# Kernel tuning notes

Measured on AMD Instinct MI355X. Metric: run time of the kernel, lower is better.

Reference implementation:

```python
import jax, jax.numpy as jnp
import numpy as np

N_NODES = 100000
N_EDGES = 1600000
F_IN = 128
HID = 64
N_LAYERS = 4
N_GRAPHS = 512
N_CLASSES = 10
BN_EPS = 1e-5


def setup_inputs() -> dict:
    key = jax.random.key(0)
    ks = jax.random.split(key, 24)
    inp = {
        "x": jax.random.normal(ks[0], (N_NODES, F_IN), dtype=jnp.float32),
        "edge_index": jax.random.randint(ks[1], (2, N_EDGES), 0, N_NODES, dtype=jnp.int32),
        "batch": jnp.sort(jax.random.randint(ks[2], (N_NODES,), 0, N_GRAPHS, dtype=jnp.int32)),
        # GINConv eps (train_eps=True, init 0) per layer
        "eps": jnp.zeros((N_LAYERS,), dtype=jnp.float32),
        # layer 0 MLP (in=F_IN)
        "W1_0": jax.random.normal(ks[3], (F_IN, HID)) * 0.05,
        "b1_0": jnp.zeros((HID,)),
        "g_0": jnp.ones((HID,)),
        "be_0": jnp.zeros((HID,)),
        "W2_0": jax.random.normal(ks[4], (HID, HID)) * 0.05,
        "b2_0": jnp.zeros((HID,)),
        # layers 1..3 MLPs stacked (in=HID)
        "W1_r": jax.random.normal(ks[5], (N_LAYERS - 1, HID, HID)) * 0.05,
        "b1_r": jnp.zeros((N_LAYERS - 1, HID)),
        "g_r": jnp.ones((N_LAYERS - 1, HID)),
        "be_r": jnp.zeros((N_LAYERS - 1, HID)),
        "W2_r": jax.random.normal(ks[6], (N_LAYERS - 1, HID, HID)) * 0.05,
        "b2_r": jnp.zeros((N_LAYERS - 1, HID)),
        # head
        "lin1_W": jax.random.normal(ks[7], (N_LAYERS * HID, HID)) * 0.05,
        "lin1_b": jnp.zeros((HID,)),
        "bn_g": jnp.ones((HID,)),
        "bn_b": jnp.zeros((HID,)),
        "lin2_W": jax.random.normal(ks[8], (HID, N_CLASSES)) * 0.05,
        "lin2_b": jnp.zeros((N_CLASSES,)),
    }
    return inp


def _bn(h, g, b):
    # BatchNorm1d training-mode math: biased variance over the batch dim
    mu = h.mean(axis=0)
    var = h.var(axis=0)
    return (h - mu) * jax.lax.rsqrt(var + BN_EPS) * g + b


def _gin_conv(x, src, dst, eps, W1, b1, g, be, W2, b2):
    # sum of neighbor (source) features scattered to target nodes
    agg = jax.ops.segment_sum(x[src], dst, num_segments=N_NODES)
    h = (1.0 + eps) * x + agg
    h = jax.nn.relu(_bn(h @ W1 + b1, g, be))
    h = jax.nn.relu(h @ W2 + b2)
    return h


def reference(x, edge_index, batch, eps,
              W1_0, b1_0, g_0, be_0, W2_0, b2_0,
              W1_r, b1_r, g_r, be_r, W2_r, b2_r,
              lin1_W, lin1_b, bn_g, bn_b, lin2_W, lin2_b):
    src, dst = edge_index[0], edge_index[1]
    h = _gin_conv(x, src, dst, eps[0], W1_0, b1_0, g_0, be_0, W2_0, b2_0)
    xs = [h]
    for i in range(N_LAYERS - 1):
        h = _gin_conv(h, src, dst, eps[i + 1], W1_r[i], b1_r[i], g_r[i], be_r[i], W2_r[i], b2_r[i])
        xs.append(h)
    hcat = jnp.concatenate(xs, axis=-1)                      # [N, L*HID]
    pooled = jax.ops.segment_sum(hcat, batch, num_segments=N_GRAPHS)  # [G, L*HID]
    out = pooled @ lin1_W + lin1_b
    out = jax.nn.relu(_bn(out, bn_g, bn_b))
    # dropout: eval mode (identity)
    out = out @ lin2_W + lin2_b
    return jax.nn.log_softmax(out, axis=-1)
```

## Files before the change

kernel.cpp:

```cpp
#include <hip/hip_runtime.h>

#define N_NODES 100000
#define N_EDGES 1600000
#define F_IN 128
#define HID 64
#define NLAYERS 4
#define N_GRAPHS 512
#define N_CLASSES 10

#define NB_BUCKET 256
#define NODES_PER_BUCKET 391
#define NBLK 256
#define EDGES_PER_BLK (N_EDGES / NBLK)

typedef unsigned int uint_t;
typedef unsigned short ushort_t;

__device__ __forceinline__ float lo_bf(uint_t w) { return __uint_as_float(w << 16); }
__device__ __forceinline__ float hi_bf(uint_t w) { return __uint_as_float(w & 0xffff0000u); }
__device__ __forceinline__ ushort_t f2bf(float f) {
    uint_t u = __float_as_uint(f);
    u += 0x7fffu + ((u >> 16) & 1u);
    return (ushort_t)(u >> 16);
}
__device__ __forceinline__ uint_t pack2(float a, float b) {
    return ((uint_t)f2bf(b) << 16) | (uint_t)f2bf(a);
}

__global__ __launch_bounds__(256) void k_zero(int* __restrict__ btotal,
                                              float* __restrict__ statsA,
                                              float* __restrict__ pooled) {
    int i = blockIdx.x * 256 + threadIdx.x;
    if (i < NB_BUCKET) btotal[i] = 0;
    if (i < NLAYERS * 128) statsA[i] = 0.f;
    if (i < N_GRAPHS * 256) pooled[i] = 0.f;
}

__global__ __launch_bounds__(512) void kb_hist(const int* __restrict__ dst,
                                               int* __restrict__ partial,
                                               int* __restrict__ btotal) {
    __shared__ int h[NB_BUCKET];
    int tid = threadIdx.x;
    if (tid < NB_BUCKET) h[tid] = 0;
    __syncthreads();
    int e0 = blockIdx.x * EDGES_PER_BLK;
    for (int i = tid; i < EDGES_PER_BLK; i += 512) {
        uint_t d = (uint_t)dst[e0 + i];
        if (d >= (uint_t)N_NODES) d = N_NODES - 1;
        atomicAdd(&h[d / NODES_PER_BUCKET], 1);
    }
    __syncthreads();
    if (tid < NB_BUCKET) {
        int c = h[tid];
        partial[blockIdx.x * NB_BUCKET + tid] = c;
        if (c) atomicAdd(&btotal[tid], c);
    }
}

__global__ __launch_bounds__(256) void kb_base(const int* __restrict__ btotal,
                                               int* __restrict__ bbase) {
    __shared__ int sh[NB_BUCKET];
    int tid = threadIdx.x;
    sh[tid] = btotal[tid];
    __syncthreads();
    for (int off = 1; off < NB_BUCKET; off <<= 1) {
        int t = (tid >= off) ? sh[tid - off] : 0;
        __syncthreads();
        sh[tid] += t;
        __syncthreads();
    }
    bbase[tid + 1] = sh[tid];
    if (tid == 0) bbase[0] = 0;
}

__global__ __launch_bounds__(256) void kb_scan(const int* __restrict__ partial,
                                               const int* __restrict__ bbase,
                                               int* __restrict__ goff) {
    __shared__ int sh[NBLK];
    int b = blockIdx.x, tid = threadIdx.x;
    sh[tid] = partial[tid * NB_BUCKET + b];
    __syncthreads();
    for (int off = 1; off < NBLK; off <<= 1) {
        int t = (tid >= off) ? sh[tid - off] : 0;
        __syncthreads();
        sh[tid] += t;
        __syncthreads();
    }
    int excl = (tid == 0) ? 0 : sh[tid - 1];
    goff[tid * NB_BUCKET + b] = bbase[b] + excl;
}

__global__ __launch_bounds__(512) void kb_scatter(const int* __restrict__ src,
                                                  const int* __restrict__ dst,
                                                  const int* __restrict__ goff,
                                                  int* __restrict__ ebuf) {
    __shared__ int cur[NB_BUCKET];
    int tid = threadIdx.x;
    if (tid < NB_BUCKET) cur[tid] = goff[blockIdx.x * NB_BUCKET + tid];
    __syncthreads();
    int e0 = blockIdx.x * EDGES_PER_BLK;
    for (int i = tid; i < EDGES_PER_BLK; i += 512) {
        uint_t d = (uint_t)dst[e0 + i];
        if (d >= (uint_t)N_NODES) d = N_NODES - 1;
        uint_t s = (uint_t)src[e0 + i];
        if (s >= (uint_t)N_NODES) s = 0;
        int b = (int)(d / NODES_PER_BUCKET);
        int dl = (int)d - b * NODES_PER_BUCKET;
        int pos = atomicAdd(&cur[b], 1);
        ebuf[pos] = (dl << 17) | (int)s;
    }
}

__global__ __launch_bounds__(512) void kb_csr(const int* __restrict__ ebuf,
                                              const int* __restrict__ bbase,
                                              int* __restrict__ row_ptr,
                                              int* __restrict__ col_src) {
    __shared__ int cnt[512];
    __shared__ int sh[512];
    __shared__ int off[512];
    int tid = threadIdx.x, b = blockIdx.x;
    int s0 = bbase[b], s1 = bbase[b + 1];
    int n = s1 - s0;
    cnt[tid] = 0;
    __syncthreads();
    for (int i = tid; i < n; i += 512) {
        int dl = ebuf[s0 + i] >> 17;
        atomicAdd(&cnt[dl], 1);
    }
    __syncthreads();
    sh[tid] = cnt[tid];
    __syncthreads();
    for (int o = 1; o < 512; o <<= 1) {
        int t = (tid >= o) ? sh[tid - o] : 0;
        __syncthreads();
        sh[tid] += t;
        __syncthreads();
    }
    off[tid] = (tid == 0) ? 0 : sh[tid - 1];
    cnt[tid] = 0;

    int node0 = b * NODES_PER_BUCKET;
    int ncnt = N_NODES - node0;
    if (ncnt > NODES_PER_BUCKET) ncnt = NODES_PER_BUCKET;
    if (tid < ncnt) row_ptr[node0 + tid] = s0 + off[tid];
    if (b == NB_BUCKET - 1 && tid == 0) row_ptr[N_NODES] = N_EDGES;
    __syncthreads();

    for (int i = tid; i < n; i += 512) {
        int v = ebuf[s0 + i];
        int dl = v >> 17;
        int r = atomicAdd(&cnt[dl], 1);
        col_src[s0 + off[dl] + r] = v & 0x1FFFF;
    }
}

__global__ __launch_bounds__(256) void k_aggregate_u(const uint2* __restrict__ y2,
                                                     const int* __restrict__ row_ptr,
                                                     const int* __restrict__ col_src,
                                                     const float* __restrict__ eps, int layer,
                                                     const float* __restrict__ b1,
                                                     uint2* __restrict__ u2) {
    int wid = threadIdx.x >> 6, lane = threadIdx.x & 63;
    int gid = lane >> 4, l4 = lane & 15;
    float one_eps = 1.0f + eps[layer];
    int stride = gridDim.x * 4;

    for (int node = blockIdx.x * 4 + wid; node < N_NODES; node += stride) {
        int e0 = row_ptr[node], e1 = row_ptr[node + 1];
        if (e0 < 0) e0 = 0;
        if (e1 > N_EDGES) e1 = N_EDGES;
        if (e1 < e0) e1 = e0;

        float4 a0 = {0.f, 0.f, 0.f, 0.f}, a1 = a0, a2 = a0, a3 = a0;

        for (int ebase = e0; ebase < e1; ebase += 64) {
            int len = e1 - ebase; if (len > 64) len = 64;
            int ci = ebase + lane; if (ci > e1 - 1) ci = e1 - 1;
            int sv = col_src[ci];
            sv = (int)min((uint_t)sv, (uint_t)(N_NODES - 1));

            int nfull = len >> 2;
            int rem = len & 3;
            int j = 0;
            for (; j + 4 <= nfull; j += 4) {
                int s0 = __shfl(sv, (j + 0) * 4 + gid, 64);
                int s1 = __shfl(sv, (j + 1) * 4 + gid, 64);
                int s2 = __shfl(sv, (j + 2) * 4 + gid, 64);
                int s3 = __shfl(sv, (j + 3) * 4 + gid, 64);
                uint2 w0 = y2[(size_t)s0 * 16 + l4];
                uint2 w1 = y2[(size_t)s1 * 16 + l4];
                uint2 w2 = y2[(size_t)s2 * 16 + l4];
                uint2 w3 = y2[(size_t)s3 * 16 + l4];
                a0.x += lo_bf(w0.x); a0.y += hi_bf(w0.x); a0.z += lo_bf(w0.y); a0.w += hi_bf(w0.y);
                a1.x += lo_bf(w1.x); a1.y += hi_bf(w1.x); a1.z += lo_bf(w1.y); a1.w += hi_bf(w1.y);
                a2.x += lo_bf(w2.x); a2.y += hi_bf(w2.x); a2.z += lo_bf(w2.y); a2.w += hi_bf(w2.y);
                a3.x += lo_bf(w3.x); a3.y += hi_bf(w3.x); a3.z += lo_bf(w3.y); a3.w += hi_bf(w3.y);
            }
            for (; j < nfull; ++j) {
                int s = __shfl(sv, j * 4 + gid, 64);
                uint2 w = y2[(size_t)s * 16 + l4];
                a0.x += lo_bf(w.x); a0.y += hi_bf(w.x); a0.z += lo_bf(w.y); a0.w += hi_bf(w.y);
            }
            if (rem) {
                int s = __shfl(sv, nfull * 4 + gid, 64);
                if (gid < rem) {
                    uint2 w = y2[(size_t)s * 16 + l4];
                    a1.x += lo_bf(w.x); a1.y += hi_bf(w.x); a1.z += lo_bf(w.y); a1.w += hi_bf(w.y);
                }
            }
        }

        float4 t;
        t.x = (a0.x + a1.x) + (a2.x + a3.x);
        t.y = (a0.y + a1.y) + (a2.y + a3.y);
        t.z = (a0.z + a1.z) + (a2.z + a3.z);
        t.w = (a0.w + a1.w) + (a2.w + a3.w);
        t.x += __shfl_xor(t.x, 16, 64); t.x += __shfl_xor(t.x, 32, 64);
        t.y += __shfl_xor(t.y, 16, 64); t.y += __shfl_xor(t.y, 32, 64);
        t.z += __shfl_xor(t.z, 16, 64); t.z += __shfl_xor(t.z, 32, 64);
        t.w += __shfl_xor(t.w, 16, 64); t.w += __shfl_xor(t.w, 32, 64);

        if (gid == 0) {
            uint2 ws = y2[(size_t)node * 16 + l4];
            float4 bb = *(const float4*)&b1[4 * l4];
            float ox = t.x + one_eps * lo_bf(ws.x) + bb.x;
            float oy = t.y + one_eps * hi_bf(ws.x) + bb.y;
            float oz = t.z + one_eps * lo_bf(ws.y) + bb.z;
            float ow = t.w + one_eps * hi_bf(ws.y) + bb.w;
            uint2 o2;
            o2.x = pack2(ox, oy);
            o2.y = pack2(oz, ow);
            u2[(size_t)node * 16 + l4] = o2;
        }
    }
}

template <int K>
__global__ __launch_bounds__(256) void k_gemm1(const float* __restrict__ A,
                                               const float* __restrict__ W,
                                               ushort_t* __restrict__ out) {
    constexpr int KP = K + 4;
    constexpr int KQ = K / 4;
    __shared__ float Al[64 * KP];
    __shared__ float Wl[K * 64];
    int tid = threadIdx.x;
    int base = blockIdx.x * 64;

    for (int i = tid; i < K * 16; i += 256)
        ((float4*)Wl)[i] = ((const float4*)W)[i];

    if (base + 64 <= N_NODES) {
        const float4* Ag = (const float4*)(A + (size_t)base * K);
        for (int i = tid; i < 16 * K; i += 256) {
            int row = i / KQ, kk = (i % KQ) * 4;
            float4 v = Ag[i];
            *(float4*)&Al[row * KP + kk] = v;
        }
    } else {
        for (int i = tid; i < 16 * K; i += 256) {
            int row = i / KQ, kk = (i % KQ) * 4;
            int grow = base + row; if (grow >= N_NODES) grow = N_NODES - 1;
            float4 v = ((const float4*)(A + (size_t)grow * K))[i % KQ];
            *(float4*)&Al[row * KP + kk] = v;
        }
    }
    __syncthreads();

    int ct = (tid & 15) * 4;
    int rb = (tid >> 4) * 4;
    float4 acc0 = {0.f, 0.f, 0.f, 0.f}, acc1 = acc0, acc2 = acc0, acc3 = acc0;
    const float* A0 = &Al[(rb + 0) * KP];
    const float* A1 = &Al[(rb + 1) * KP];
    const float* A2 = &Al[(rb + 2) * KP];
    const float* A3 = &Al[(rb + 3) * KP];
    #pragma unroll 4
    for (int k = 0; k < K; ++k) {
        float4 w = *(const float4*)&Wl[k * 64 + ct];
        float a0 = A0[k], a1 = A1[k], a2 = A2[k], a3 = A3[k];
        acc0.x = fmaf(a0, w.x, acc0.x); acc0.y = fmaf(a0, w.y, acc0.y);
        acc0.z = fmaf(a0, w.z, acc0.z); acc0.w = fmaf(a0, w.w, acc0.w);
        acc1.x = fmaf(a1, w.x, acc1.x); acc1.y = fmaf(a1, w.y, acc1.y);
        acc1.z = fmaf(a1, w.z, acc1.z); acc1.w = fmaf(a1, w.w, acc1.w);
        acc2.x = fmaf(a2, w.x, acc2.x); acc2.y = fmaf(a2, w.y, acc2.y);
        acc2.z = fmaf(a2, w.z, acc2.z); acc2.w = fmaf(a2, w.w, acc2.w);
        acc3.x = fmaf(a3, w.x, acc3.x); acc3.y = fmaf(a3, w.y, acc3.y);
        acc3.z = fmaf(a3, w.z, acc3.z); acc3.w = fmaf(a3, w.w, acc3.w);
    }

    float4 accs[4] = {acc0, acc1, acc2, acc3};
    #pragma unroll
    for (int r = 0; r < 4; ++r) {
        int row = base + rb + r;
        if (row < N_NODES) {
            ushort4 o;
            o.x = f2bf(accs[r].x); o.y = f2bf(accs[r].y);
            o.z = f2bf(accs[r].z); o.w = f2bf(accs[r].w);
            *(ushort4*)&out[(size_t)row * 64 + ct] = o;
        }
    }
}

template <bool NEXT>
__global__ __launch_bounds__(256) void k_fused(const uint2* __restrict__ U2,
                                               const float* __restrict__ W2,
                                               const float* __restrict__ sums,
                                               const float* __restrict__ g_,
                                               const float* __restrict__ be,
                                               const float* __restrict__ b2,
                                               const int* __restrict__ batch,
                                               float* __restrict__ pooled, int layer,
                                               const float* __restrict__ W1n,
                                               ushort_t* __restrict__ ynext) {
    constexpr int K = 64, KP = 68, KQ = 16;
    __shared__ float Al[64 * KP];
    __shared__ float Wl[K * 64];
    __shared__ float W1l[NEXT ? K * 64 : 4];
    __shared__ float Pl[256];
    __shared__ __align__(16) float Sc[64];
    __shared__ __align__(16) float Sh[64];
    int tid = threadIdx.x;
    int base = blockIdx.x * 64;

    if (tid < 64) {
        const float inv_n = 1.0f / N_NODES;
        float mean = sums[tid] * inv_n;
        float var = sums[64 + tid] * inv_n - mean * mean;
        if (var < 0.f) var = 0.f;
        float inv = rsqrtf(var + 1e-5f);
        float sc = inv * g_[tid];
        Sc[tid] = sc;
        Sh[tid] = be[tid] - mean * sc;
    }
    for (int i = tid; i < K * 16; i += 256)
        ((float4*)Wl)[i] = ((const float4*)W2)[i];
    if (NEXT) {
        for (int i = tid; i < K * 16; i += 256)
            ((float4*)W1l)[i] = ((const float4*)W1n)[i];
    }
    __syncthreads();

    {
        bool full = (base + 64 <= N_NODES);
        for (int i = tid; i < 16 * K; i += 256) {
            int row = i / KQ, kq = i % KQ, kk = kq * 4;
            int grow = base + row;
            if (!full && grow >= N_NODES) grow = N_NODES - 1;
            uint2 w = U2[(size_t)grow * 16 + kq];
            float4 v = {lo_bf(w.x), hi_bf(w.x), lo_bf(w.y), hi_bf(w.y)};
            float4 sc = *(const float4*)&Sc[kk];
            float4 sh = *(const float4*)&Sh[kk];
            v.x = fmaxf(fmaf(v.x, sc.x, sh.x), 0.f);
            v.y = fmaxf(fmaf(v.y, sc.y, sh.y), 0.f);
            v.z = fmaxf(fmaf(v.z, sc.z, sh.z), 0.f);
            v.w = fmaxf(fmaf(v.w, sc.w, sh.w), 0.f);
            *(float4*)&Al[row * KP + kk] = v;
        }
    }
    __syncthreads();

    int ct = (tid & 15) * 4;
    int rb = (tid >> 4) * 4;
    float4 acc0 = {0.f, 0.f, 0.f, 0.f}, acc1 = acc0, acc2 = acc0, acc3 = acc0;
    {
        const float* A0 = &Al[(rb + 0) * KP];
        const float* A1 = &Al[(rb + 1) * KP];
        const float* A2 = &Al[(rb + 2) * KP];
        const float* A3 = &Al[(rb + 3) * KP];
        #pragma unroll 4
        for (int k = 0; k < K; ++k) {
            float4 w = *(const float4*)&Wl[k * 64 + ct];
            float a0 = A0[k], a1 = A1[k], a2 = A2[k], a3 = A3[k];
            acc0.x = fmaf(a0, w.x, acc0.x); acc0.y = fmaf(a0, w.y, acc0.y);
            acc0.z = fmaf(a0, w.z, acc0.z); acc0.w = fmaf(a0, w.w, acc0.w);
            acc1.x = fmaf(a1, w.x, acc1.x); acc1.y = fmaf(a1, w.y, acc1.y);
            acc1.z = fmaf(a1, w.z, acc1.z); acc1.w = fmaf(a1, w.w, acc1.w);
            acc2.x = fmaf(a2, w.x, acc2.x); acc2.y = fmaf(a2, w.y, acc2.y);
            acc2.z = fmaf(a2, w.z, acc2.z); acc2.w = fmaf(a2, w.w, acc2.w);
            acc3.x = fmaf(a3, w.x, acc3.x); acc3.y = fmaf(a3, w.y, acc3.y);
            acc3.z = fmaf(a3, w.z, acc3.z); acc3.w = fmaf(a3, w.w, acc3.w);
        }
    }
    __syncthreads();

    {
        float4 bb = *(const float4*)&b2[ct];
        float4 accs[4] = {acc0, acc1, acc2, acc3};
        #pragma unroll
        for (int r = 0; r < 4; ++r) {
            float4 o;
            o.x = fmaxf(accs[r].x + bb.x, 0.f);
            o.y = fmaxf(accs[r].y + bb.y, 0.f);
            o.z = fmaxf(accs[r].z + bb.z, 0.f);
            o.w = fmaxf(accs[r].w + bb.w, 0.f);
            *(float4*)&Al[(rb + r) * KP + ct] = o;
        }
    }
    __syncthreads();

    {
        int lastEx = base + 64; if (lastEx > N_NODES) lastEx = N_NODES;
        int gstart = batch[base];
        int gend = batch[lastEx - 1];
        if (gstart < 0) gstart = 0;
        if (gend > N_GRAPHS - 1) gend = N_GRAPHS - 1;
        int col = tid & 63, q = tid >> 6;
        int rs = base;
        for (int g = gstart; g <= gend; ++g) {
            int lo = rs, hi = lastEx;
            while (lo < hi) { int mid = (lo + hi) >> 1; if (batch[mid] <= g) lo = mid + 1; else hi = mid; }
            int re = lo;
            float s = 0.f;
            for (int r = rs + q; r < re; r += 4) s += Al[(r - base) * KP + col];
            Pl[tid] = s;
            __syncthreads();
            if (tid < 64) {
                float tot = (Pl[col] + Pl[64 + col]) + (Pl[128 + col] + Pl[192 + col]);
                atomicAdd(&pooled[g * 256 + layer * 64 + col], tot);
            }
            __syncthreads();
            rs = re;
        }
    }

    if (NEXT) {
        float4 y0 = {0.f, 0.f, 0.f, 0.f}, y1 = y0, y2_ = y0, y3 = y0;
        const float* A0 = &Al[(rb + 0) * KP];
        const float* A1 = &Al[(rb + 1) * KP];
        const float* A2 = &Al[(rb + 2) * KP];
        const float* A3 = &Al[(rb + 3) * KP];
        #pragma unroll 4
        for (int k = 0; k < K; ++k) {
            float4 w = *(const float4*)&W1l[k * 64 + ct];
            float a0 = A0[k], a1 = A1[k], a2 = A2[k], a3 = A3[k];
            y0.x = fmaf(a0, w.x, y0.x); y0.y = fmaf(a0, w.y, y0.y);
            y0.z = fmaf(a0, w.z, y0.z); y0.w = fmaf(a0, w.w, y0.w);
            y1.x = fmaf(a1, w.x, y1.x); y1.y = fmaf(a1, w.y, y1.y);
            y1.z = fmaf(a1, w.z, y1.z); y1.w = fmaf(a1, w.w, y1.w);
            y2_.x = fmaf(a2, w.x, y2_.x); y2_.y = fmaf(a2, w.y, y2_.y);
            y2_.z = fmaf(a2, w.z, y2_.z); y2_.w = fmaf(a2, w.w, y2_.w);
            y3.x = fmaf(a3, w.x, y3.x); y3.y = fmaf(a3, w.y, y3.y);
            y3.z = fmaf(a3, w.z, y3.z); y3.w = fmaf(a3, w.w, y3.w);
        }
        float4 ys[4] = {y0, y1, y2_, y3};
        #pragma unroll
        for (int r = 0; r < 4; ++r) {
            int row = base + rb + r;
            if (row < N_NODES) {
                ushort4 o;
                o.x = f2bf(ys[r].x); o.y = f2bf(ys[r].y);
                o.z = f2bf(ys[r].z); o.w = f2bf(ys[r].w);
                *(ushort4*)&ynext[(size_t)row * 64 + ct] = o;
            }
        }
    }
}

__global__ __launch_bounds__(256) void k_stats(const uint2* __restrict__ u2, float* __restrict__ sums) {
    __shared__ float sh[256 * 8];
    int tid = threadIdx.x;
    float a[4] = {0.f, 0.f, 0.f, 0.f}, b[4] = {0.f, 0.f, 0.f, 0.f};
    for (size_t i = (size_t)blockIdx.x * 256 + tid; i < (size_t)N_NODES * 16; i += (size_t)gridDim.x * 256) {
        uint2 w = u2[i];
        float v0 = lo_bf(w.x), v1 = hi_bf(w.x), v2 = lo_bf(w.y), v3 = hi_bf(w.y);
        a[0] += v0; b[0] += v0 * v0;
        a[1] += v1; b[1] += v1 * v1;
        a[2] += v2; b[2] += v2 * v2;
        a[3] += v3; b[3] += v3 * v3;
    }
    #pragma unroll
    for (int j = 0; j < 4; ++j) { sh[tid * 8 + j] = a[j]; sh[tid * 8 + 4 + j] = b[j]; }
    __syncthreads();
    if (tid < 64) {
        int quad = tid >> 2, o = tid & 3;
        float s = 0.f, ss = 0.f;
        for (int g = 0; g < 16; ++g) {
            int t = g * 16 + quad;
            s  += sh[t * 8 + o];
            ss += sh[t * 8 + 4 + o];
        }
        atomicAdd(&sums[tid], s);
        atomicAdd(&sums[64 + tid], ss);
    }
}

__global__ __launch_bounds__(64) void k_head1(const float* __restrict__ pooled,
                                              const float* __restrict__ W, const float* __restrict__ b,
                                              float* __restrict__ t1) {
    __shared__ __align__(16) float pl[256];
    int g = blockIdx.x, lane = threadIdx.x;
    ((float4*)pl)[lane] = ((const float4*)(pooled + g * 256))[lane];
    __syncthreads();
    float acc = b[lane];
    for (int k = 0; k < 256; ++k) acc += pl[k] * W[k * 64 + lane];
    t1[g * 64 + lane] = acc;
}

__global__ __launch_bounds__(64) void k_head3(const float* __restrict__ t1,
                                              const float* __restrict__ g_, const float* __restrict__ b_,
                                              const float* __restrict__ W2, const float* __restrict__ b2,
                                              float* __restrict__ out) {
    __shared__ float v[64];
    __shared__ float o[16];
    int g = blockIdx.x, lane = threadIdx.x;
    float s = 0.f, q = 0.f;
    for (int r = 0; r < N_GRAPHS; ++r) {
        float vv = t1[r * 64 + lane];
        s += vv; q += vv * vv;
    }
    float mean = s * (1.0f / N_GRAPHS);
    float var = q * (1.0f / N_GRAPHS) - mean * mean;
    if (var < 0.f) var = 0.f;
    float inv = rsqrtf(var + 1e-5f);
    float sc = inv * g_[lane];
    float sh = b_[lane] - mean * sc;
    float x = t1[g * 64 + lane] * sc + sh;
    v[lane] = fmaxf(x, 0.f);
    __syncthreads();
    if (lane < N_CLASSES) {
        float acc = b2[lane];
        for (int k = 0; k < 64; ++k) acc += v[k] * W2[k * N_CLASSES + lane];
        o[lane] = acc;
    }
    __syncthreads();
    if (lane < N_CLASSES) {
        float m = -1e30f;
        for (int k = 0; k < N_CLASSES; ++k) m = fmaxf(m, o[k]);
        float ssum = 0.f;
        for (int k = 0; k < N_CLASSES; ++k) ssum += expf(o[k] - m);
        out[g * N_CLASSES + lane] = o[lane] - m - logf(ssum);
    }
}

extern "C" void kernel_launch(void* const* d_in, const int* in_sizes, int n_in,
                              void* d_out, int out_size, void* d_ws, size_t ws_size,
                              hipStream_t stream) {
    const float* x      = (const float*)d_in[0];
    const int*   ei     = (const int*)d_in[1];
    const int*   srcArr = ei;
    const int*   dstArr = ei + N_EDGES;
    const int*   batch  = (const int*)d_in[2];
    const float* eps    = (const float*)d_in[3];
    const float* W1_0   = (const float*)d_in[4];
    const float* b1_0   = (const float*)d_in[5];
    const float* g_0    = (const float*)d_in[6];
    const float* be_0   = (const float*)d_in[7];
    const float* W2_0   = (const float*)d_in[8];
    const float* b2_0   = (const float*)d_in[9];
    const float* W1_r   = (const float*)d_in[10];
    const float* b1_r   = (const float*)d_in[11];
    const float* g_r    = (const float*)d_in[12];
    const float* be_r   = (const float*)d_in[13];
    const float* W2_r   = (const float*)d_in[14];
    const float* b2_r   = (const float*)d_in[15];
    const float* lin1W  = (const float*)d_in[16];
    const float* lin1b  = (const float*)d_in[17];
    const float* bn_g   = (const float*)d_in[18];
    const float* bn_b   = (const float*)d_in[19];
    const float* lin2W  = (const float*)d_in[20];
    const float* lin2b  = (const float*)d_in[21];

    char* ws = (char*)d_ws;
    auto alloc = [&](size_t bytes) {
        char* p = ws;
        ws += (bytes + 255) & ~(size_t)255;
        return p;
    };
    int*      row_ptr = (int*)alloc(((size_t)N_NODES + 1) * 4);
    int*      col_src = (int*)alloc((size_t)N_EDGES * 4);
    int*      ebuf    = (int*)alloc((size_t)N_EDGES * 4);
    int*      partial = (int*)alloc((size_t)NBLK * NB_BUCKET * 4);
    int*      goff    = (int*)alloc((size_t)NBLK * NB_BUCKET * 4);
    int*      btotal  = (int*)alloc((size_t)NB_BUCKET * 4);
    int*      bbase   = (int*)alloc(((size_t)NB_BUCKET + 1) * 4);
    ushort_t* ybf     = (ushort_t*)alloc((size_t)N_NODES * 64 * 2);
    ushort_t* ubf     = (ushort_t*)alloc((size_t)N_NODES * 64 * 2);
    float*    statsA  = (float*)alloc(NLAYERS * 128 * 4);
    float*    pooled  = (float*)alloc((size_t)N_GRAPHS * 256 * 4);
    float*    t1      = (float*)alloc((size_t)N_GRAPHS * 64 * 4);

    k_zero<<<(N_GRAPHS * 256 + 255) / 256, 256, 0, stream>>>(btotal, statsA, pooled);
    kb_hist<<<NBLK, 512, 0, stream>>>(dstArr, partial, btotal);
    kb_base<<<1, 256, 0, stream>>>(btotal, bbase);
    kb_scan<<<NB_BUCKET, 256, 0, stream>>>(partial, bbase, goff);
    kb_scatter<<<NBLK, 512, 0, stream>>>(srcArr, dstArr, goff, ebuf);
    kb_csr<<<NB_BUCKET, 512, 0, stream>>>(ebuf, bbase, row_ptr, col_src);

    const int agg_blocks = 2048;
    const int gemm_grid = (N_NODES + 63) / 64;

    k_gemm1<128><<<gemm_grid, 256, 0, stream>>>(x, W1_0, ybf);

    for (int l = 0; l < NLAYERS; ++l) {
        const float *b1, *gg, *be, *W2, *b2;
        if (l == 0) { b1 = b1_0; gg = g_0; be = be_0; W2 = W2_0; b2 = b2_0; }
        else {
            b1 = b1_r + (size_t)(l - 1) * 64;
            gg = g_r  + (size_t)(l - 1) * 64;
            be = be_r + (size_t)(l - 1) * 64;
            W2 = W2_r + (size_t)(l - 1) * 64 * 64;
            b2 = b2_r + (size_t)(l - 1) * 64;
        }
        k_aggregate_u<<<agg_blocks, 256, 0, stream>>>((const uint2*)ybf, row_ptr, col_src, eps, l, b1,
                                                      (uint2*)ubf);
        k_stats<<<512, 256, 0, stream>>>((const uint2*)ubf, statsA + l * 128);
        if (l < NLAYERS - 1) {
            const float* W1n = W1_r + (size_t)l * 64 * 64;
            k_fused<true><<<gemm_grid, 256, 0, stream>>>((const uint2*)ubf, W2, statsA + l * 128, gg, be, b2,
                                                         batch, pooled, l, W1n, ybf);
        } else {
            k_fused<false><<<gemm_grid, 256, 0, stream>>>((const uint2*)ubf, W2, statsA + l * 128, gg, be, b2,
                                                          batch, pooled, l, nullptr, nullptr);
        }
    }

    k_head1<<<N_GRAPHS, 64, 0, stream>>>(pooled, lin1W, lin1b, t1);
    k_head3<<<N_GRAPHS, 64, 0, stream>>>(t1, bn_g, bn_b, lin2W, lin2b, (float*)d_out);
}
```

Baseline: 562.6 us.

## Fuse BN stats into aggregation and make fused MLP kernel persistent

Batch-norm sum and sum-of-squares are now accumulated inside the aggregation kernel from the rounded bf16 outputs. Each block writes its partials to a transposed buffer that reuses ebuf, and a small k_redstats kernel reduces them. This removes the separate k_stats pass over the whole activation array and its global atomics. The fused MLP kernel becomes a grid-stride loop over 64-row tiles with a fixed grid of 1024, sharing one weight smem buffer for W2 and W1n, which cuts LDS use but reloads the weights on every tile.

```diff
diff --git a/kernel.cpp b/kernel.cpp
--- a/kernel.cpp
+++ b/kernel.cpp
@@ -12,6 +12,10 @@
 #define NODES_PER_BUCKET 391
 #define NBLK 256
 #define EDGES_PER_BLK (N_EDGES / NBLK)
+
+#define N_TILES ((N_NODES + 63) / 64)
+#define FUSED_GRID 1024
+#define NAGG 2048
 
 typedef unsigned int uint_t;
 typedef unsigned short ushort_t;
@@ -159,11 +163,17 @@
                                                      const int* __restrict__ col_src,
                                                      const float* __restrict__ eps, int layer,
                                                      const float* __restrict__ b1,
-                                                     uint2* __restrict__ u2) {
-    int wid = threadIdx.x >> 6, lane = threadIdx.x & 63;
+                                                     uint2* __restrict__ u2,
+                                                     float* __restrict__ partialsT) {
+    __shared__ float red[512];
+    int tid = threadIdx.x;
+    int wid = tid >> 6, lane = tid & 63;
     int gid = lane >> 4, l4 = lane & 15;
     float one_eps = 1.0f + eps[layer];
     int stride = gridDim.x * 4;
+
+    float4 ss = {0.f, 0.f, 0.f, 0.f};
+    float4 sq = {0.f, 0.f, 0.f, 0.f};
 
     for (int node = blockIdx.x * 4 + wid; node < N_NODES; node += stride) {
         int e0 = row_ptr[node], e1 = row_ptr[node + 1];
@@ -231,8 +241,42 @@
             o2.x = pack2(ox, oy);
             o2.y = pack2(oz, ow);
             u2[(size_t)node * 16 + l4] = o2;
-        }
-    }
+            float q0 = lo_bf(o2.x), q1 = hi_bf(o2.x), q2 = lo_bf(o2.y), q3 = hi_bf(o2.y);
+            ss.x += q0; ss.y += q1; ss.z += q2; ss.w += q3;
+            sq.x += q0 * q0; sq.y += q1 * q1; sq.z += q2 * q2; sq.w += q3 * q3;
+        }
+    }
+
+    if (gid == 0) {
+        int off = (wid * 16 + l4) * 8;
+        red[off + 0] = ss.x; red[off + 1] = ss.y; red[off + 2] = ss.z; red[off + 3] = ss.w;
+        red[off + 4] = sq.x; red[off + 5] = sq.y; red[off + 6] = sq.z; red[off + 7] = sq.w;
+    }
+    __syncthreads();
+    if (tid < 128) {
+        int sel = tid >> 6, c = tid & 63;
+        int l4i = c >> 2, j = c & 3;
+        float v = red[(0 * 16 + l4i) * 8 + sel * 4 + j]
+                + red[(1 * 16 + l4i) * 8 + sel * 4 + j]
+                + red[(2 * 16 + l4i) * 8 + sel * 4 + j]
+                + red[(3 * 16 + l4i) * 8 + sel * 4 + j];
+        partialsT[(size_t)(sel * 64 + c) * NAGG + blockIdx.x] = v;
+    }
+}
+
+__global__ __launch_bounds__(256) void k_redstats(const float* __restrict__ pT,
+                                                  float* __restrict__ outp) {
+    __shared__ float sh[256];
+    int b = blockIdx.x, tid = threadIdx.x;
+    float v = 0.f;
+    for (int i = tid; i < NAGG; i += 256) v += pT[(size_t)b * NAGG + i];
+    sh[tid] = v;
+    __syncthreads();
+    for (int off = 128; off > 0; off >>= 1) {
+        if (tid < off) sh[tid] += sh[tid + off];
+        __syncthreads();
+    }
+    if (tid == 0) outp[b] = sh[0];
 }
 
 template <int K>
@@ -314,12 +358,10 @@
     constexpr int K = 64, KP = 68, KQ = 16;
     __shared__ float Al[64 * KP];
     __shared__ float Wl[K * 64];
-    __shared__ float W1l[NEXT ? K * 64 : 4];
     __shared__ float Pl[256];
     __shared__ __align__(16) float Sc[64];
     __shared__ __align__(16) float Sh[64];
     int tid = threadIdx.x;
-    int base = blockIdx.x * 64;
 
     if (tid < 64) {
         const float inv_n = 1.0f / N_NODES;
@@ -331,155 +373,133 @@
         Sc[tid] = sc;
         Sh[tid] = be[tid] - mean * sc;
     }
-    for (int i = tid; i < K * 16; i += 256)
-        ((float4*)Wl)[i] = ((const float4*)W2)[i];
-    if (NEXT) {
-        for (int i = tid; i < K * 16; i += 256)
-            ((float4*)W1l)[i] = ((const float4*)W1n)[i];
-    }
-    __syncthreads();
-
-    {
-        bool full = (base + 64 <= N_NODES);
-        for (int i = tid; i < 16 * K; i += 256) {
-            int row = i / KQ, kq = i % KQ, kk = kq * 4;
-            int grow = base + row;
-            if (!full && grow >= N_NODES) grow = N_NODES - 1;
-            uint2 w = U2[(size_t)grow * 16 + kq];
-            float4 v = {lo_bf(w.x), hi_bf(w.x), lo_bf(w.y), hi_bf(w.y)};
-            float4 sc = *(const float4*)&Sc[kk];
-            float4 sh = *(const float4*)&Sh[kk];
-            v.x = fmaxf(fmaf(v.x, sc.x, sh.x), 0.f);
-            v.y = fmaxf(fmaf(v.y, sc.y, sh.y), 0.f);
-            v.z = fmaxf(fmaf(v.z, sc.z, sh.z), 0.f);
-            v.w = fmaxf(fmaf(v.w, sc.w, sh.w), 0.f);
-            *(float4*)&Al[row * KP + kk] = v;
-        }
-    }
     __syncthreads();
 
     int ct = (tid & 15) * 4;
     int rb = (tid >> 4) * 4;
-    float4 acc0 = {0.f, 0.f, 0.f, 0.f}, acc1 = acc0, acc2 = acc0, acc3 = acc0;
-    {
-        const float* A0 = &Al[(rb + 0) * KP];
-        const float* A1 = &Al[(rb + 1) * KP];
-        const float* A2 = &Al[(rb + 2) * KP];
-        const float* A3 = &Al[(rb + 3) * KP];
-        #pragma unroll 4
-        for (int k = 0; k < K; ++k) {
-            float4 w = *(const float4*)&Wl[k * 64 + ct];
-            float a0 = A0[k], a1 = A1[k], a2 = A2[k], a3 = A3[k];
-            acc0.x = fmaf(a0, w.x, acc0.x); acc0.y = fmaf(a0, w.y, acc0.y);
-            acc0.z = fmaf(a0, w.z, acc0.z); acc0.w = fmaf(a0, w.w, acc0.w);
-            acc1.x = fmaf(a1, w.x, acc1.x); acc1.y = fmaf(a1, w.y, acc1.y);
-            acc1.z = fmaf(a1, w.z, acc1.z); acc1.w = fmaf(a1, w.w, acc1.w);
-            acc2.x = fmaf(a2, w.x, acc2.x); acc2.y = fmaf(a2, w.y, acc2.y);
-            acc2.z = fmaf(a2, w.z, acc2.z); acc2.w = fmaf(a2, w.w, acc2.w);
-            acc3.x = fmaf(a3, w.x, acc3.x); acc3.y = fmaf(a3, w.y, acc3.y);
-            acc3.z = fmaf(a3, w.z, acc3.z); acc3.w = fmaf(a3, w.w, acc3.w);
-        }
-    }
-    __syncthreads();
-
-    {
-        float4 bb = *(const float4*)&b2[ct];
-        float4 accs[4] = {acc0, acc1, acc2, acc3};
-        #pragma unroll
-        for (int r = 0; r < 4; ++r) {
-            float4 o;
-            o.x = fmaxf(accs[r].x + bb.x, 0.f);
-            o.y = fmaxf(accs[r].y + bb.y, 0.f);
-            o.z = fmaxf(accs[r].z + bb.z, 0.f);
-            o.w = fmaxf(accs[r].w + bb.w, 0.f);
-            *(float4*)&Al[(rb + r) * KP + ct] = o;
-        }
-    }
-    __syncthreads();
-
-    {
-        int lastEx = base + 64; if (lastEx > N_NODES) lastEx = N_NODES;
-        int gstart = batch[base];
-        int gend = batch[lastEx - 1];
-        if (gstart < 0) gstart = 0;
-        if (gend > N_GRAPHS - 1) gend = N_GRAPHS - 1;
-        int col = tid & 63, q = tid >> 6;
-        int rs = base;
-        for (int g = gstart; g <= gend; ++g) {
-            int lo = rs, hi = lastEx;
-            while (lo < hi) { int mid = (lo + hi) >> 1; if (batch[mid] <= g) lo = mid + 1; else hi = mid; }
-            int re = lo;
-            float s = 0.f;
-            for (int r = rs + q; r < re; r += 4) s += Al[(r - base) * KP + col];
-            Pl[tid] = s;
-            __syncthreads();
-            if (tid < 64) {
-                float tot = (Pl[col] + Pl[64 + col]) + (Pl[128 + col] + Pl[192 + col]);
-                atomicAdd(&pooled[g * 256 + layer * 64 + col], tot);
-            }
-            __syncthreads();
-            rs = re;
-        }
-    }
-
-    if (NEXT) {
-        float4 y0 = {0.f, 0.f, 0.f, 0.f}, y1 = y0, y2_ = y0, y3 = y0;
-        const float* A0 = &Al[(rb + 0) * KP];
-        const float* A1 = &Al[(rb + 1) * KP];
-        const float* A2 = &Al[(rb + 2) * KP];
-        const float* A3 = &Al[(rb + 3) * KP];
-        #pragma unroll 4
-        for (int k = 0; k < K; ++k) {
-            float4 w = *(const float4*)&W1l[k * 64 + ct];
-            float a0 = A0[k], a1 = A1[k], a2 = A2[k], a3 = A3[k];
-            y0.x = fmaf(a0, w.x, y0.x); y0.y = fmaf(a0, w.y, y0.y);
-            y0.z = fmaf(a0, w.z, y0.z); y0.w = fmaf(a0, w.w, y0.w);
-            y1.x = fmaf(a1, w.x, y1.x); y1.y = fmaf(a1, w.y, y1.y);
-            y1.z = fmaf(a1, w.z, y1.z); y1.w = fmaf(a1, w.w, y1.w);
-            y2_.x = fmaf(a2, w.x, y2_.x); y2_.y = fmaf(a2, w.y, y2_.y);
-            y2_.z = fmaf(a2, w.z, y2_.z); y2_.w = fmaf(a2, w.w, y2_.w);
-            y3.x = fmaf(a3, w.x, y3.x); y3.y = fmaf(a3, w.y, y3.y);
-            y3.z = fmaf(a3, w.z, y3.z); y3.w = fmaf(a3, w.w, y3.w);
-        }
-        float4 ys[4] = {y0, y1, y2_, y3};
-        #pragma unroll
-        for (int r = 0; r < 4; ++r) {
-            int row = base + rb + r;
-            if (row < N_NODES) {
-                ushort4 o;
-                o.x = f2bf(ys[r].x); o.y = f2bf(ys[r].y);
-                o.z = f2bf(ys[r].z); o.w = f2bf(ys[r].w);
-                *(ushort4*)&ynext[(size_t)row * 64 + ct] = o;
-            }
-        }
-    }
-}
-
-__global__ __launch_bounds__(256) void k_stats(const uint2* __restrict__ u2, float* __restrict__ sums) {
-    __shared__ float sh[256 * 8];
-    int tid = threadIdx.x;
-    float a[4] = {0.f, 0.f, 0.f, 0.f}, b[4] = {0.f, 0.f, 0.f, 0.f};
-    for (size_t i = (size_t)blockIdx.x * 256 + tid; i < (size_t)N_NODES * 16; i += (size_t)gridDim.x * 256) {
-        uint2 w = u2[i];
-        float v0 = lo_bf(w.x), v1 = hi_bf(w.x), v2 = lo_bf(w.y), v3 = hi_bf(w.y);
-        a[0] += v0; b[0] += v0 * v0;
-        a[1] += v1; b[1] += v1 * v1;
-        a[2] += v2; b[2] += v2 * v2;
-        a[3] += v3; b[3] += v3 * v3;
-    }
-    #pragma unroll
-    for (int j = 0; j < 4; ++j) { sh[tid * 8 + j] = a[j]; sh[tid * 8 + 4 + j] = b[j]; }
-    __syncthreads();
-    if (tid < 64) {
-        int quad = tid >> 2, o = tid & 3;
-        float s = 0.f, ss = 0.f;
-        for (int g = 0; g < 16; ++g) {
-            int t = g * 16 + quad;
-            s  += sh[t * 8 + o];
-            ss += sh[t * 8 + 4 + o];
-        }
-        atomicAdd(&sums[tid], s);
-        atomicAdd(&sums[64 + tid], ss);
+
+    for (int tile = blockIdx.x; tile < N_TILES; tile += gridDim.x) {
+        int base = tile * 64;
+
+        for (int i = tid; i < K * 16; i += 256)
+            ((float4*)Wl)[i] = ((const float4*)W2)[i];
+        {
+            bool full = (base + 64 <= N_NODES);
+            for (int i = tid; i < 16 * K; i += 256) {
+                int row = i / KQ, kq = i % KQ, kk = kq * 4;
+                int grow = base + row;
+                if (!full && grow >= N_NODES) grow = N_NODES - 1;
+                uint2 w = U2[(size_t)grow * 16 + kq];
+                float4 v = {lo_bf(w.x), hi_bf(w.x), lo_bf(w.y), hi_bf(w.y)};
+                float4 sc = *(const float4*)&Sc[kk];
+                float4 sh = *(const float4*)&Sh[kk];
+                v.x = fmaxf(fmaf(v.x, sc.x, sh.x), 0.f);
+                v.y = fmaxf(fmaf(v.y, sc.y, sh.y), 0.f);
+                v.z = fmaxf(fmaf(v.z, sc.z, sh.z), 0.f);
+                v.w = fmaxf(fmaf(v.w, sc.w, sh.w), 0.f);
+                *(float4*)&Al[row * KP + kk] = v;
+            }
+        }
+        __syncthreads();
+
+        float4 acc0 = {0.f, 0.f, 0.f, 0.f}, acc1 = acc0, acc2 = acc0, acc3 = acc0;
+        {
+            const float* A0 = &Al[(rb + 0) * KP];
+            const float* A1 = &Al[(rb + 1) * KP];
+            const float* A2 = &Al[(rb + 2) * KP];
+            const float* A3 = &Al[(rb + 3) * KP];
+            #pragma unroll 4
+            for (int k = 0; k < K; ++k) {
+                float4 w = *(const float4*)&Wl[k * 64 + ct];
+                float a0 = A0[k], a1 = A1[k], a2 = A2[k], a3 = A3[k];
+                acc0.x = fmaf(a0, w.x, acc0.x); acc0.y = fmaf(a0, w.y, acc0.y);
+                acc0.z = fmaf(a0, w.z, acc0.z); acc0.w = fmaf(a0, w.w, acc0.w);
+                acc1.x = fmaf(a1, w.x, acc1.x); acc1.y = fmaf(a1, w.y, acc1.y);
+                acc1.z = fmaf(a1, w.z, acc1.z); acc1.w = fmaf(a1, w.w, acc1.w);
+                acc2.x = fmaf(a2, w.x, acc2.x); acc2.y = fmaf(a2, w.y, acc2.y);
+                acc2.z = fmaf(a2, w.z, acc2.z); acc2.w = fmaf(a2, w.w, acc2.w);
+                acc3.x = fmaf(a3, w.x, acc3.x); acc3.y = fmaf(a3, w.y, acc3.y);
+                acc3.z = fmaf(a3, w.z, acc3.z); acc3.w = fmaf(a3, w.w, acc3.w);
+            }
+        }
+        __syncthreads();
+
+        {
+            float4 bb = *(const float4*)&b2[ct];
+            float4 accs[4] = {acc0, acc1, acc2, acc3};
+            #pragma unroll
+            for (int r = 0; r < 4; ++r) {
+                float4 o;
+                o.x = fmaxf(accs[r].x + bb.x, 0.f);
+                o.y = fmaxf(accs[r].y + bb.y, 0.f);
+                o.z = fmaxf(accs[r].z + bb.z, 0.f);
+                o.w = fmaxf(accs[r].w + bb.w, 0.f);
+                *(float4*)&Al[(rb + r) * KP + ct] = o;
+            }
+        }
+        if (NEXT) {
+            for (int i = tid; i < K * 16; i += 256)
+                ((float4*)Wl)[i] = ((const float4*)W1n)[i];
+        }
+        __syncthreads();
+
+        if (NEXT) {
+            float4 y0 = {0.f, 0.f, 0.f, 0.f}, y1 = y0, y2_ = y0, y3 = y0;
+            const float* A0 = &Al[(rb + 0) * KP];
+            const float* A1 = &Al[(rb + 1) * KP];
+            const float* A2 = &Al[(rb + 2) * KP];
+            const float* A3 = &Al[(rb + 3) * KP];
+            #pragma unroll 4
+            for (int k = 0; k < K; ++k) {
+                float4 w = *(const float4*)&Wl[k * 64 + ct];
+                float a0 = A0[k], a1 = A1[k], a2 = A2[k], a3 = A3[k];
+                y0.x = fmaf(a0, w.x, y0.x); y0.y = fmaf(a0, w.y, y0.y);
+                y0.z = fmaf(a0, w.z, y0.z); y0.w = fmaf(a0, w.w, y0.w);
+                y1.x = fmaf(a1, w.x, y1.x); y1.y = fmaf(a1, w.y, y1.y);
+                y1.z = fmaf(a1, w.z, y1.z); y1.w = fmaf(a1, w.w, y1.w);
+                y2_.x = fmaf(a2, w.x, y2_.x); y2_.y = fmaf(a2, w.y, y2_.y);
+                y2_.z = fmaf(a2, w.z, y2_.z); y2_.w = fmaf(a2, w.w, y2_.w);
+                y3.x = fmaf(a3, w.x, y3.x); y3.y = fmaf(a3, w.y, y3.y);
+                y3.z = fmaf(a3, w.z, y3.z); y3.w = fmaf(a3, w.w, y3.w);
+            }
+            float4 ys[4] = {y0, y1, y2_, y3};
+            #pragma unroll
+            for (int r = 0; r < 4; ++r) {
+                int row = base + rb + r;
+                if (row < N_NODES) {
+                    ushort4 o;
+                    o.x = f2bf(ys[r].x); o.y = f2bf(ys[r].y);
+                    o.z = f2bf(ys[r].z); o.w = f2bf(ys[r].w);
+                    *(ushort4*)&ynext[(size_t)row * 64 + ct] = o;
+                }
+            }
+        }
+
+        {
+            int lastEx = base + 64; if (lastEx > N_NODES) lastEx = N_NODES;
+            int gstart = batch[base];
+            int gend = batch[lastEx - 1];
+            if (gstart < 0) gstart = 0;
+            if (gend > N_GRAPHS - 1) gend = N_GRAPHS - 1;
+            int col = tid & 63, q = tid >> 6;
+            int rs = base;
+            for (int g = gstart; g <= gend; ++g) {
+                int lo = rs, hi = lastEx;
+                while (lo < hi) { int mid = (lo + hi) >> 1; if (batch[mid] <= g) lo = mid + 1; else hi = mid; }
+                int re = lo;
+                float s = 0.f;
+                for (int r = rs + q; r < re; r += 4) s += Al[(r - base) * KP + col];
+                Pl[tid] = s;
+                __syncthreads();
+                if (tid < 64) {
+                    float tot = (Pl[col] + Pl[64 + col]) + (Pl[128 + col] + Pl[192 + col]);
+                    atomicAdd(&pooled[g * 256 + layer * 64 + col], tot);
+                }
+                __syncthreads();
+                rs = re;
+            }
+        }
+        __syncthreads();
     }
 }
 
@@ -565,18 +585,19 @@
         ws += (bytes + 255) & ~(size_t)255;
         return p;
     };
-    int*      row_ptr = (int*)alloc(((size_t)N_NODES + 1) * 4);
-    int*      col_src = (int*)alloc((size_t)N_EDGES * 4);
-    int*      ebuf    = (int*)alloc((size_t)N_EDGES * 4);
-    int*      partial = (int*)alloc((size_t)NBLK * NB_BUCKET * 4);
-    int*      goff    = (int*)alloc((size_t)NBLK * NB_BUCKET * 4);
-    int*      btotal  = (int*)alloc((size_t)NB_BUCKET * 4);
-    int*      bbase   = (int*)alloc(((size_t)NB_BUCKET + 1) * 4);
-    ushort_t* ybf     = (ushort_t*)alloc((size_t)N_NODES * 64 * 2);
-    ushort_t* ubf     = (ushort_t*)alloc((size_t)N_NODES * 64 * 2);
-    float*    statsA  = (float*)alloc(NLAYERS * 128 * 4);
-    float*    pooled  = (float*)alloc((size_t)N_GRAPHS * 256 * 4);
-    float*    t1      = (float*)alloc((size_t)N_GRAPHS * 64 * 4);
+    int*      row_ptr  = (int*)alloc(((size_t)N_NODES + 1) * 4);
+    int*      col_src  = (int*)alloc((size_t)N_EDGES * 4);
+    int*      ebuf     = (int*)alloc((size_t)N_EDGES * 4);
+    int*      partial  = (int*)alloc((size_t)NBLK * NB_BUCKET * 4);
+    int*      goff     = (int*)alloc((size_t)NBLK * NB_BUCKET * 4);
+    int*      btotal   = (int*)alloc((size_t)NB_BUCKET * 4);
+    int*      bbase    = (int*)alloc(((size_t)NB_BUCKET + 1) * 4);
+    ushort_t* ybf      = (ushort_t*)alloc((size_t)N_NODES * 64 * 2);
+    ushort_t* ubf      = (ushort_t*)alloc((size_t)N_NODES * 64 * 2);
+    float*    statsA   = (float*)alloc(NLAYERS * 128 * 4);
+    float*    pooled   = (float*)alloc((size_t)N_GRAPHS * 256 * 4);
+    float*    t1       = (float*)alloc((size_t)N_GRAPHS * 64 * 4);
+    float*    partialsT = (float*)ebuf;
 
     k_zero<<<(N_GRAPHS * 256 + 255) / 256, 256, 0, stream>>>(btotal, statsA, pooled);
     kb_hist<<<NBLK, 512, 0, stream>>>(dstArr, partial, btotal);
@@ -585,7 +606,6 @@
     kb_scatter<<<NBLK, 512, 0, stream>>>(srcArr, dstArr, goff, ebuf);
     kb_csr<<<NB_BUCKET, 512, 0, stream>>>(ebuf, bbase, row_ptr, col_src);
 
-    const int agg_blocks = 2048;
     const int gemm_grid = (N_NODES + 63) / 64;
 
     k_gemm1<128><<<gemm_grid, 256, 0, stream>>>(x, W1_0, ybf);
@@ -600,16 +620,16 @@
             W2 = W2_r + (size_t)(l - 1) * 64 * 64;
             b2 = b2_r + (size_t)(l - 1) * 64;
         }
-        k_aggregate_u<<<agg_blocks, 256, 0, stream>>>((const uint2*)ybf, row_ptr, col_src, eps, l, b1,
-                                                      (uint2*)ubf);
-        k_stats<<<512, 256, 0, stream>>>((const uint2*)ubf, statsA + l * 128);
+        k_aggregate_u<<<NAGG, 256, 0, stream>>>((const uint2*)ybf, row_ptr, col_src, eps, l, b1,
+                                                (uint2*)ubf, partialsT);
+        k_redstats<<<128, 256, 0, stream>>>(partialsT, statsA + l * 128);
         if (l < NLAYERS - 1) {
             const float* W1n = W1_r + (size_t)l * 64 * 64;
-            k_fused<true><<<gemm_grid, 256, 0, stream>>>((const uint2*)ubf, W2, statsA + l * 128, gg, be, b2,
-                                                         batch, pooled, l, W1n, ybf);
+            k_fused<true><<<FUSED_GRID, 256, 0, stream>>>((const uint2*)ubf, W2, statsA + l * 128, gg, be, b2,
+                                                          batch, pooled, l, W1n, ybf);
         } else {
-            k_fused<false><<<gemm_grid, 256, 0, stream>>>((const uint2*)ubf, W2, statsA + l * 128, gg, be, b2,
-                                                          batch, pooled, l, nullptr, nullptr);
+            k_fused<false><<<FUSED_GRID, 256, 0, stream>>>((const uint2*)ubf, W2, statsA + l * 128, gg, be, b2,
+                                                           batch, pooled, l, nullptr, nullptr);
         }
     }
 
```

Result: slower. 604.0 us (+7.3%).
